# Optimization experiments

Measured on AMD Instinct MI355X. Metric: run time of the kernel, lower is better.

The kernel has to match this reference:

```python
import jax, jax.numpy as jnp
import numpy as np

DT_NS = 8.0
ALPHA, BETA, GAMMA, RISE_W = 0.7, 0.2, 0.1, 0.05
DECAY_TAUS = jnp.array([40.0, 300.0, 230.0, 2.4], dtype=jnp.float32)
RISE_TAUS = jnp.array([5.0, 20.0, 10.0, 2.0], dtype=jnp.float32)
TAIL = 195  # tail window: [peak+5, peak+200)


def setup_inputs() -> dict:
    key = jax.random.key(0)
    k1, k2, k3, k4 = jax.random.split(key, 4)
    B, S, C = 32768, 1024, 4
    return {
        "logits": jax.random.normal(k1, (B, C), dtype=jnp.float32),
        "labels": jax.random.randint(k2, (B,), 0, C, dtype=jnp.int64),
        "waveforms": jax.random.uniform(k3, (B, S), dtype=jnp.float32),
        "amplitudes": jax.random.uniform(k4, (B,), dtype=jnp.float32),
    }


def _masked_mean(vals, valid):
    w = valid.astype(vals.dtype)
    n = jnp.sum(w)
    return jnp.where(n > 0, jnp.sum(vals * w) / jnp.maximum(n, 1.0), 0.0)


def _decay_time_loss(waveforms, pred_cls):
    B, S = waveforms.shape
    peak = jnp.argmax(waveforms, axis=1)                      # (B,)
    valid = peak < S - 20
    # fixed-size tail window starting at peak+5, masked past end of record
    idx = peak[:, None] + 5 + jnp.arange(TAIL)[None, :]       # (B, TAIL)
    in_range = idx < S
    tail = jnp.take_along_axis(waveforms, jnp.minimum(idx, S - 1), axis=1)
    pos = in_range & (tail > 0)                               # positive-sample mask
    w = pos.astype(jnp.float32)
    n_pos = jnp.sum(w, axis=1)
    valid &= n_pos >= 5
    t = (jnp.arange(TAIL, dtype=jnp.float32) * DT_NS)[None, :]
    log_tail = jnp.log(jnp.where(pos, tail, 1.0) + 1e-8)
    n_safe = jnp.maximum(n_pos, 1.0)
    t_mean = jnp.sum(w * t, axis=1) / n_safe
    y_mean = jnp.sum(w * log_tail, axis=1) / n_safe
    dt_c = t - t_mean[:, None]
    num = jnp.sum(w * dt_c * (log_tail - y_mean[:, None]), axis=1)
    den = jnp.sum(w * dt_c * dt_c, axis=1)
    valid &= den > 0
    slope = num / jnp.maximum(den, 1e-30)
    fitted_tau = -1.0 / (slope + 1e-8)
    tau_loss = (fitted_tau - DECAY_TAUS[pred_cls]) ** 2
    return _masked_mean(tau_loss, valid)


def _energy_conservation_loss(waveforms, amplitudes):
    charge = jnp.sum(jnp.maximum(waveforms, 0.0), axis=1)
    ratio = charge / (amplitudes + 1e-8)
    return jnp.var(ratio, ddof=1)  # torch.var default is unbiased


def _rise_time_loss(waveforms, pred_cls):
    B, S = waveforms.shape
    peak = jnp.argmax(waveforms, axis=1)
    amp = jnp.take_along_axis(waveforms, peak[:, None], axis=1)[:, 0]
    valid = peak >= 10
    edge = jnp.arange(S)[None, :] < peak[:, None]             # rising edge mask
    ab10 = edge & (waveforms >= 0.1 * amp[:, None])
    ab90 = edge & (waveforms >= 0.9 * amp[:, None])
    valid &= jnp.any(ab10, axis=1) & jnp.any(ab90, axis=1)
    idx10 = jnp.argmax(ab10, axis=1).astype(jnp.float32)      # first crossing
    idx90 = jnp.argmax(ab90, axis=1).astype(jnp.float32)
    rise = (idx90 - idx10) * DT_NS
    exp_rise = RISE_TAUS[pred_cls]
    rt_loss = jnp.abs(rise - exp_rise) / exp_rise
    return _masked_mean(rt_loss, valid)


def reference(logits, labels, waveforms, amplitudes):
    logp = jax.nn.log_softmax(logits, axis=-1)
    ce = -jnp.mean(jnp.take_along_axis(logp, labels[:, None], axis=1)[:, 0])
    pred_cls = jnp.argmax(logits, axis=1)
    decay = _decay_time_loss(waveforms, pred_cls)
    energy = _energy_conservation_loss(waveforms, amplitudes)
    rise = _rise_time_loss(waveforms, pred_cls)
    total = ALPHA * ce + BETA * decay + GAMMA * energy + RISE_W * rise
    return total, ce, decay, energy, rise
```

## Files before the change

kernel.cpp:

```cpp
#include <hip/hip_runtime.h>
#include <cmath>

#define BROWS 32768
#define SLEN  1024
#define TAILW 195
#define NB1   8192
#define NB2   128
#define PSTRIDE 128

__device__ __constant__ float c_decay_taus[4] = {40.0f, 300.0f, 230.0f, 2.4f};
__device__ __constant__ float c_rise_taus[4]  = {5.0f, 20.0f, 10.0f, 2.0f};

typedef float v2f __attribute__((ext_vector_type(2)));

struct alignas(16) RowStat {
    unsigned nSk;
    unsigned Skk;
    float    csum;
    unsigned pki;
    double   Sy;
    double   Sky;
};

template<int CTRL>
__device__ __forceinline__ unsigned dpp0_u32(unsigned x) {
    return (unsigned)__builtin_amdgcn_update_dpp(0, (int)x, CTRL, 0xf, 0xf, true);
}
template<int CTRL>
__device__ __forceinline__ float dpp0_f32(float x) {
    return __int_as_float(
        __builtin_amdgcn_update_dpp(0, __float_as_int(x), CTRL, 0xf, 0xf, true));
}
template<int CTRL>
__device__ __forceinline__ float dppid_f32(float x) {
    return __int_as_float(__builtin_amdgcn_update_dpp(
        __float_as_int(x), __float_as_int(x), CTRL, 0xf, 0xf, false));
}
template<int CTRL>
__device__ __forceinline__ double dpp0_f64(double x) {
    const int lo = __builtin_amdgcn_update_dpp(0, __double2loint(x), CTRL, 0xf, 0xf, true);
    const int hi = __builtin_amdgcn_update_dpp(0, __double2hiint(x), CTRL, 0xf, 0xf, true);
    return __hiloint2double(hi, lo);
}
#define ROW_SHR1  0x111
#define ROW_SHR2  0x112
#define ROW_SHR4  0x114
#define ROW_SHR8  0x118
#define BCAST15   0x142
#define BCAST31   0x143
#define WSUM_F32(x) { x += dpp0_f32<ROW_SHR1>(x); x += dpp0_f32<ROW_SHR2>(x); \
                      x += dpp0_f32<ROW_SHR4>(x); x += dpp0_f32<ROW_SHR8>(x); \
                      x += dpp0_f32<BCAST15>(x);  x += dpp0_f32<BCAST31>(x); }
#define WSUM_U32(x) { x += dpp0_u32<ROW_SHR1>(x); x += dpp0_u32<ROW_SHR2>(x); \
                      x += dpp0_u32<ROW_SHR4>(x); x += dpp0_u32<ROW_SHR8>(x); \
                      x += dpp0_u32<BCAST15>(x);  x += dpp0_u32<BCAST31>(x); }
#define WSUM_F64(x) { x += dpp0_f64<ROW_SHR1>(x); x += dpp0_f64<ROW_SHR2>(x); \
                      x += dpp0_f64<ROW_SHR4>(x); x += dpp0_f64<ROW_SHR8>(x); \
                      x += dpp0_f64<BCAST15>(x);  x += dpp0_f64<BCAST31>(x); }
#define WMAX_F32(x) { x = fmaxf(x, dppid_f32<ROW_SHR1>(x)); x = fmaxf(x, dppid_f32<ROW_SHR2>(x)); \
                      x = fmaxf(x, dppid_f32<ROW_SHR4>(x)); x = fmaxf(x, dppid_f32<ROW_SHR8>(x)); \
                      x = fmaxf(x, dppid_f32<BCAST15>(x));  x = fmaxf(x, dppid_f32<BCAST31>(x)); }

extern "C" __global__ __launch_bounds__(256, 8)
void physics_rows(const float* __restrict__ wave, RowStat* __restrict__ stats)
{
    const int lane = threadIdx.x & 63;
    const int row  = (blockIdx.x * 256 + (int)threadIdx.x) >> 6;
    const int lane4 = lane * 4;
    const float4* p = reinterpret_cast<const float4*>(wave) + (size_t)row * (SLEN / 4) + lane;

    const float4 c0 = p[0], c1 = p[64], c2 = p[128], c3 = p[192];
    float vals[16] = {c0.x,c0.y,c0.z,c0.w, c1.x,c1.y,c1.z,c1.w,
                      c2.x,c2.y,c2.z,c2.w, c3.x,c3.y,c3.z,c3.w};

    float m0 = fmaxf(fmaxf(vals[0],  vals[1]),  vals[2]);
    float m1 = fmaxf(fmaxf(vals[3],  vals[4]),  vals[5]);
    float m2 = fmaxf(fmaxf(vals[6],  vals[7]),  vals[8]);
    float m3 = fmaxf(fmaxf(vals[9],  vals[10]), vals[11]);
    float m4 = fmaxf(fmaxf(vals[12], vals[13]), fmaxf(vals[14], vals[15]));
    float bm = fmaxf(fmaxf(fmaxf(m0, m1), m2), fmaxf(m3, m4));

    v2f sa = {0.f, 0.f}, sb = {0.f, 0.f};
    #pragma unroll
    for (int k = 0; k < 16; k += 4) {
        v2f p0 = {vals[k],     vals[k + 1]};
        v2f p1 = {vals[k + 2], vals[k + 3]};
        sa += __builtin_elementwise_max(p0, (v2f){0.f, 0.f});
        sb += __builtin_elementwise_max(p1, (v2f){0.f, 0.f});
    }
    const v2f sab = sa + sb;
    float csum = sab.x + sab.y;

    WMAX_F32(bm);
    WSUM_F32(csum);
    const float amp = __int_as_float(
        __builtin_amdgcn_readlane(__float_as_int(bm), 63));

    int peak = SLEN;
    #pragma unroll
    for (int q = 0; q < 4; ++q) {
        bool found = false;
        #pragma unroll
        for (int r = 0; r < 4; ++r) {
            const unsigned long long b = __ballot(vals[q * 4 + r] == amp);
            if (b) {
                peak = min(peak, q * 256 + 4 * (__ffsll(b) - 1) + r);
                found = true;
            }
        }
        if (found) break;
    }
    peak = __builtin_amdgcn_readfirstlane(peak);
    const bool do_decay = (peak < SLEN - 20);
    const int  pm5 = peak + 5;

    const float t10v = 0.1f * amp, t90v = 0.9f * amp;
    int i10 = SLEN, i90 = SLEN;
    const int q_peak = peak >> 8;
    #pragma unroll
    for (int q = 0; q < 4; ++q) {
        if (q > q_peak || (i10 < SLEN && i90 < SLEN)) break;
        const int qb = q * 256;
        unsigned long long m10[4], m90[4];
        #pragma unroll
        for (int r = 0; r < 4; ++r) {
            m10[r] = __ballot(vals[q * 4 + r] >= t10v);
            m90[r] = __ballot(vals[q * 4 + r] >= t90v);
        }
        if (q == q_peak) {
            #pragma unroll
            for (int r = 0; r < 4; ++r) {
                const int cnt = (peak - qb - r + 3) >> 2;
                const unsigned long long lm =
                    (cnt >= 64) ? ~0ull : ((cnt <= 0) ? 0ull : ((1ull << cnt) - 1ull));
                m10[r] &= lm; m90[r] &= lm;
            }
        }
        if (i10 == SLEN) {
            int best = SLEN;
            #pragma unroll
            for (int r = 0; r < 4; ++r)
                if (m10[r]) best = min(best, qb + 4 * (__ffsll(m10[r]) - 1) + r);
            i10 = best;
        }
        if (i90 == SLEN) {
            int best = SLEN;
            #pragma unroll
            for (int r = 0; r < 4; ++r)
                if (m90[r]) best = min(best, qb + 4 * (__ffsll(m90[r]) - 1) + r);
            i90 = best;
        }
    }

    double Sy = 0.0, Sky = 0.0;
    int cnt = 0;
    if (do_decay) {
        #pragma unroll
        for (int q = 0; q < 4; ++q) {
            if (q * 256 + 255 >= pm5 && q * 256 <= pm5 + (TAILW - 1)) {
                #pragma unroll
                for (int r = 0; r < 4; ++r) {
                    const int kk = q * 256 + lane4 + r - pm5;
                    const float w = vals[q * 4 + r];
                    const bool cond = ((unsigned)kk < (unsigned)TAILW) && (w > 0.0f);
                    const float ym = cond ? __logf(w + 1e-8f) : 0.0f;
                    cnt += (int)__popcll(__ballot(cond));
                    const double y64 = (double)ym;
                    Sy += y64;
                    Sky = fma((double)kk, y64, Sky);
                }
            }
        }
    }
    WSUM_F64(Sy);
    WSUM_F64(Sky);

    unsigned out_nSk = 0, out_Skk = 0;
    if (do_decay) {
        const int L = min(TAILW, SLEN - pm5);
        if (cnt == (int)L) {
            const unsigned uL = (unsigned)L;
            const unsigned Sk = uL * (uL - 1u) / 2u;
            out_nSk = uL | (Sk << 16);
            out_Skk = (uL - 1u) * uL * (2u * uL - 1u) / 6u;
        } else {
            unsigned nSk_p = 0, Skk = 0;
            #pragma unroll
            for (int q = 0; q < 4; ++q) {
                if (q * 256 + 255 >= pm5 && q * 256 <= pm5 + (TAILW - 1)) {
                    #pragma unroll
                    for (int r = 0; r < 4; ++r) {
                        const int kk = q * 256 + lane4 + r - pm5;
                        const float w = vals[q * 4 + r];
                        if (((unsigned)kk < (unsigned)TAILW) && (w > 0.0f)) {
                            nSk_p += 1u + ((unsigned)kk << 8);
                            Skk   += (unsigned)(kk * kk);
                        }
                    }
                }
            }
            WSUM_U32(nSk_p);
            WSUM_U32(Skk);
            out_nSk = (nSk_p & 0xFFu) | ((nSk_p >> 8) << 16);
            out_Skk = Skk;
        }
    }

    if (lane == 63) {
        RowStat st;
        st.nSk  = out_nSk;
        st.Skk  = out_Skk;
        st.csum = csum;
        st.pki  = ((unsigned)peak << 22) | ((unsigned)i10 << 11) | (unsigned)i90;
        st.Sy   = Sy;
        st.Sky  = Sky;
        stats[row] = st;
    }
}

extern "C" __global__ __launch_bounds__(256)
void physics_rowfin(const RowStat* __restrict__ stats,
                    const float* __restrict__ logits,
                    const int* __restrict__ labels,
                    const float* __restrict__ amps,
                    double* __restrict__ partials,
                    unsigned* __restrict__ counter,
                    float* __restrict__ out)
{
    const int r    = blockIdx.x * 256 + threadIdx.x;
    const int lane = threadIdx.x & 63;
    const int wid  = threadIdx.x >> 6;

    __shared__ double sm[4][7];
    __shared__ int s_last;

    const RowStat st = stats[r];
    const unsigned n_u  = st.nSk & 0xFFFFu;
    const unsigned Sk_u = st.nSk >> 16;
    const int peak = (int)(st.pki >> 22);
    const int i10  = (int)((st.pki >> 11) & 0x7FFu);
    const int i90  = (int)(st.pki & 0x7FFu);

    const float4 l4 = reinterpret_cast<const float4*>(logits)[r];
    float lg[4] = {l4.x, l4.y, l4.z, l4.w};
    int pred = 0; float pbest = lg[0];
    #pragma unroll
    for (int c = 1; c < 4; ++c) if (lg[c] > pbest) { pbest = lg[c]; pred = c; }
    const float m = fmaxf(fmaxf(lg[0], lg[1]), fmaxf(lg[2], lg[3]));
    const float sexp = expf(lg[0] - m) + expf(lg[1] - m)
                     + expf(lg[2] - m) + expf(lg[3] - m);
    const float lse = m + logf(sexp);
    const double v0 = (double)(lse - lg[labels[r]]);

    double v1 = 0.0, v2 = 0.0;
    if (peak < SLEN - 20 && n_u >= 5u) {
        const double dn  = (double)n_u;
        const double dSk = (double)Sk_u;
        const double num = st.Sky - dSk * st.Sy / dn;
        const double den = 8.0 * ((double)st.Skk - dSk * dSk / dn);
        if (den > 0.0) {
            const double slope = num / fmax(den, 1e-30);
            const double tau   = -1.0 / (slope + 1e-8);
            const double d     = tau - (double)c_decay_taus[pred];
            v1 = d * d; v2 = 1.0;
        }
    }
    double v3 = 0.0, v4 = 0.0;
    if (peak >= 10 && i10 < SLEN && i90 < SLEN) {
        const float rise = (float)(i90 - i10) * 8.0f;
        const float er   = c_rise_taus[pred];
        v3 = (double)(fabsf(rise - er) / er); v4 = 1.0;
    }
    const double ratio = (double)st.csum / ((double)amps[r] + 1e-8);

    double v[7] = {v0, v1, v2, v3, v4, ratio, ratio * ratio};
    #pragma unroll
    for (int i = 0; i < 7; ++i) {
        #pragma unroll
        for (int off = 1; off < 64; off <<= 1)
            v[i] += __shfl_xor(v[i], off, 64);
    }
    if (lane == 0) {
        #pragma unroll
        for (int i = 0; i < 7; ++i) sm[wid][i] = v[i];
    }
    __syncthreads();
    if (threadIdx.x < 7) {
        const int i = threadIdx.x;
        const double t = sm[0][i] + sm[1][i] + sm[2][i] + sm[3][i];
        __hip_atomic_store(&partials[(size_t)i * PSTRIDE + blockIdx.x], t,
                           __ATOMIC_RELAXED, __HIP_MEMORY_SCOPE_AGENT);
    }
    __syncthreads();
    if (threadIdx.x == 0) {
        const unsigned prev = __hip_atomic_fetch_add(counter, 1u,
                                  __ATOMIC_ACQ_REL, __HIP_MEMORY_SCOPE_AGENT);
        s_last = (prev == NB2 - 1) ? 1 : 0;
    }
    __syncthreads();
    if (!s_last) return;

    double loc[7] = {0, 0, 0, 0, 0, 0, 0};
    if (threadIdx.x < PSTRIDE) {
        #pragma unroll
        for (int i = 0; i < 7; ++i)
            loc[i] = __hip_atomic_load(&partials[(size_t)i * PSTRIDE + threadIdx.x],
                                       __ATOMIC_RELAXED, __HIP_MEMORY_SCOPE_AGENT);
    }
    #pragma unroll
    for (int i = 0; i < 7; ++i) {
        #pragma unroll
        for (int off = 1; off < 64; off <<= 1)
            loc[i] += __shfl_xor(loc[i], off, 64);
    }
    __syncthreads();
    if (lane == 0 && wid < 2) {
        #pragma unroll
        for (int i = 0; i < 7; ++i) sm[wid][i] = loc[i];
    }
    __syncthreads();
    if (threadIdx.x == 0) {
        double t[7];
        #pragma unroll
        for (int i = 0; i < 7; ++i) t[i] = sm[0][i] + sm[1][i];
        const double Bn = (double)BROWS;
        const double ce    = t[0] / Bn;
        const double decay = (t[2] > 0.0) ? t[1] / fmax(t[2], 1.0) : 0.0;
        const double rise  = (t[4] > 0.0) ? t[3] / fmax(t[4], 1.0) : 0.0;
        const double var   = (t[6] - t[5] * t[5] / Bn) / (Bn - 1.0);
        const double total = 0.7 * ce + 0.2 * decay + 0.1 * var + 0.05 * rise;
        out[0] = (float)total; out[1] = (float)ce; out[2] = (float)decay;
        out[3] = (float)var;   out[4] = (float)rise;
    }
}

extern "C" void kernel_launch(void* const* d_in, const int* in_sizes, int n_in,
                              void* d_out, int out_size, void* d_ws, size_t ws_size,
                              hipStream_t stream) {
    const float* logits = (const float*)d_in[0];
    const int*   labels = (const int*)d_in[1];
    const float* wave   = (const float*)d_in[2];
    const float* amps   = (const float*)d_in[3];

    RowStat*  stats    = (RowStat*)d_ws;
    double*   partials = (double*)((char*)d_ws + (size_t)BROWS * sizeof(RowStat));
    unsigned* counter  = (unsigned*)((char*)partials + 7 * PSTRIDE * sizeof(double));

    hipMemsetAsync(counter, 0, sizeof(unsigned), stream);
    physics_rows<<<NB1, 256, 0, stream>>>(wave, stats);
    physics_rowfin<<<NB2, 256, 0, stream>>>(stats, logits, labels, amps,
                                            partials, counter, (float*)d_out);
}
```

Before: 39.74 us.

## Process two waveform rows per wavefront to interleave reductions and loads

Each wavefront now handles two rows instead of one. It issues all eight float4 loads up front and interleaves the cross-lane DPP max/sum reductions and the per-row phases of both rows, which halves the number of launched blocks. The aim is more memory-level parallelism and instruction-level overlap of the latency-bound DPP reduction chains. In exchange, register use per thread roughly doubles, and the launch bound drops from 8 to 4 waves per EU, which lowers occupancy.

```diff
diff --git a/kernel.cpp b/kernel.cpp
--- a/kernel.cpp
+++ b/kernel.cpp
@@ -4,7 +4,7 @@
 #define BROWS 32768
 #define SLEN  1024
 #define TAILW 195
-#define NB1   8192
+#define NB1   4096
 #define NB2   128
 #define PSTRIDE 128
 
@@ -61,41 +61,16 @@
                       x = fmaxf(x, dppid_f32<ROW_SHR4>(x)); x = fmaxf(x, dppid_f32<ROW_SHR8>(x)); \
                       x = fmaxf(x, dppid_f32<BCAST15>(x));  x = fmaxf(x, dppid_f32<BCAST31>(x)); }
 
-extern "C" __global__ __launch_bounds__(256, 8)
-void physics_rows(const float* __restrict__ wave, RowStat* __restrict__ stats)
+struct RowRed {
+    int peak, i10, i90, cnt;
+    double Sy, Sky;
+    unsigned nSk_p, Skk;
+    bool slow;
+};
+
+__device__ __forceinline__ void row_phase(const float (&vals)[16], float amp,
+                                          int lane4, RowRed& R)
 {
-    const int lane = threadIdx.x & 63;
-    const int row  = (blockIdx.x * 256 + (int)threadIdx.x) >> 6;
-    const int lane4 = lane * 4;
-    const float4* p = reinterpret_cast<const float4*>(wave) + (size_t)row * (SLEN / 4) + lane;
-
-    const float4 c0 = p[0], c1 = p[64], c2 = p[128], c3 = p[192];
-    float vals[16] = {c0.x,c0.y,c0.z,c0.w, c1.x,c1.y,c1.z,c1.w,
-                      c2.x,c2.y,c2.z,c2.w, c3.x,c3.y,c3.z,c3.w};
-
-    float m0 = fmaxf(fmaxf(vals[0],  vals[1]),  vals[2]);
-    float m1 = fmaxf(fmaxf(vals[3],  vals[4]),  vals[5]);
-    float m2 = fmaxf(fmaxf(vals[6],  vals[7]),  vals[8]);
-    float m3 = fmaxf(fmaxf(vals[9],  vals[10]), vals[11]);
-    float m4 = fmaxf(fmaxf(vals[12], vals[13]), fmaxf(vals[14], vals[15]));
-    float bm = fmaxf(fmaxf(fmaxf(m0, m1), m2), fmaxf(m3, m4));
-
-    v2f sa = {0.f, 0.f}, sb = {0.f, 0.f};
-    #pragma unroll
-    for (int k = 0; k < 16; k += 4) {
-        v2f p0 = {vals[k],     vals[k + 1]};
-        v2f p1 = {vals[k + 2], vals[k + 3]};
-        sa += __builtin_elementwise_max(p0, (v2f){0.f, 0.f});
-        sb += __builtin_elementwise_max(p1, (v2f){0.f, 0.f});
-    }
-    const v2f sab = sa + sb;
-    float csum = sab.x + sab.y;
-
-    WMAX_F32(bm);
-    WSUM_F32(csum);
-    const float amp = __int_as_float(
-        __builtin_amdgcn_readlane(__float_as_int(bm), 63));
-
     int peak = SLEN;
     #pragma unroll
     for (int q = 0; q < 4; ++q) {
@@ -172,19 +147,13 @@
             }
         }
     }
-    WSUM_F64(Sy);
-    WSUM_F64(Sky);
-
-    unsigned out_nSk = 0, out_Skk = 0;
+
+    unsigned nSk_p = 0, Skk = 0;
+    bool slow = false;
     if (do_decay) {
         const int L = min(TAILW, SLEN - pm5);
-        if (cnt == (int)L) {
-            const unsigned uL = (unsigned)L;
-            const unsigned Sk = uL * (uL - 1u) / 2u;
-            out_nSk = uL | (Sk << 16);
-            out_Skk = (uL - 1u) * uL * (2u * uL - 1u) / 6u;
-        } else {
-            unsigned nSk_p = 0, Skk = 0;
+        if (cnt != L) {
+            slow = true;
             #pragma unroll
             for (int q = 0; q < 4; ++q) {
                 if (q * 256 + 255 >= pm5 && q * 256 <= pm5 + (TAILW - 1)) {
@@ -199,22 +168,113 @@
                     }
                 }
             }
+        }
+    }
+    R.peak = peak; R.i10 = i10; R.i90 = i90; R.cnt = cnt;
+    R.Sy = Sy; R.Sky = Sky; R.nSk_p = nSk_p; R.Skk = Skk; R.slow = slow;
+}
+
+__device__ __forceinline__ void row_stat(const RowRed& R, float csum,
+                                         RowStat& st)
+{
+    unsigned out_nSk = 0, out_Skk = 0;
+    if (R.peak < SLEN - 20) {
+        const int L = min(TAILW, SLEN - (R.peak + 5));
+        if (!R.slow) {
+            const unsigned uL = (unsigned)L;
+            const unsigned Sk = uL * (uL - 1u) / 2u;
+            out_nSk = uL | (Sk << 16);
+            out_Skk = (uL - 1u) * uL * (2u * uL - 1u) / 6u;
+        } else {
+            unsigned nSk_p = R.nSk_p, Skk = R.Skk;
             WSUM_U32(nSk_p);
             WSUM_U32(Skk);
             out_nSk = (nSk_p & 0xFFu) | ((nSk_p >> 8) << 16);
             out_Skk = Skk;
         }
     }
+    st.nSk  = out_nSk;
+    st.Skk  = out_Skk;
+    st.csum = csum;
+    st.pki  = ((unsigned)R.peak << 22) | ((unsigned)R.i10 << 11) | (unsigned)R.i90;
+}
+
+extern "C" __global__ __launch_bounds__(256, 4)
+void physics_rows(const float* __restrict__ wave, RowStat* __restrict__ stats)
+{
+    const int lane  = threadIdx.x & 63;
+    const int gwave = (blockIdx.x * 256 + (int)threadIdx.x) >> 6;
+    const int rowA  = gwave * 2;
+    const int rowB  = rowA + 1;
+    const int lane4 = lane * 4;
+    const float4* pA = reinterpret_cast<const float4*>(wave) + (size_t)rowA * (SLEN / 4) + lane;
+    const float4* pB = pA + (SLEN / 4);
+
+    const float4 a0 = pA[0], a1 = pA[64], a2 = pA[128], a3 = pA[192];
+    const float4 b0 = pB[0], b1 = pB[64], b2 = pB[128], b3 = pB[192];
+    float vA[16] = {a0.x,a0.y,a0.z,a0.w, a1.x,a1.y,a1.z,a1.w,
+                    a2.x,a2.y,a2.z,a2.w, a3.x,a3.y,a3.z,a3.w};
+    float vB[16] = {b0.x,b0.y,b0.z,b0.w, b1.x,b1.y,b1.z,b1.w,
+                    b2.x,b2.y,b2.z,b2.w, b3.x,b3.y,b3.z,b3.w};
+
+    float amA0 = fmaxf(fmaxf(vA[0],  vA[1]),  vA[2]);
+    float bmA1 = fmaxf(fmaxf(vA[3],  vA[4]),  vA[5]);
+    float amA2 = fmaxf(fmaxf(vA[6],  vA[7]),  vA[8]);
+    float bmA3 = fmaxf(fmaxf(vA[9],  vA[10]), vA[11]);
+    float amA4 = fmaxf(fmaxf(vA[12], vA[13]), fmaxf(vA[14], vA[15]));
+    float bmA  = fmaxf(fmaxf(fmaxf(amA0, bmA1), amA2), fmaxf(bmA3, amA4));
+
+    float amB0 = fmaxf(fmaxf(vB[0],  vB[1]),  vB[2]);
+    float bmB1 = fmaxf(fmaxf(vB[3],  vB[4]),  vB[5]);
+    float amB2 = fmaxf(fmaxf(vB[6],  vB[7]),  vB[8]);
+    float bmB3 = fmaxf(fmaxf(vB[9],  vB[10]), vB[11]);
+    float amB4 = fmaxf(fmaxf(vB[12], vB[13]), fmaxf(vB[14], vB[15]));
+    float bmB  = fmaxf(fmaxf(fmaxf(amB0, bmB1), amB2), fmaxf(bmB3, amB4));
+
+    v2f saA = {0.f, 0.f}, sbA = {0.f, 0.f}, saB = {0.f, 0.f}, sbB = {0.f, 0.f};
+    #pragma unroll
+    for (int k = 0; k < 16; k += 4) {
+        v2f pa0 = {vA[k],     vA[k + 1]};
+        v2f pa1 = {vA[k + 2], vA[k + 3]};
+        v2f pb0 = {vB[k],     vB[k + 1]};
+        v2f pb1 = {vB[k + 2], vB[k + 3]};
+        saA += __builtin_elementwise_max(pa0, (v2f){0.f, 0.f});
+        sbA += __builtin_elementwise_max(pa1, (v2f){0.f, 0.f});
+        saB += __builtin_elementwise_max(pb0, (v2f){0.f, 0.f});
+        sbB += __builtin_elementwise_max(pb1, (v2f){0.f, 0.f});
+    }
+    const v2f sabA = saA + sbA;
+    const v2f sabB = saB + sbB;
+    float csumA = sabA.x + sabA.y;
+    float csumB = sabB.x + sabB.y;
+
+    WMAX_F32(bmA);
+    WMAX_F32(bmB);
+    WSUM_F32(csumA);
+    WSUM_F32(csumB);
+    const float ampA = __int_as_float(
+        __builtin_amdgcn_readlane(__float_as_int(bmA), 63));
+    const float ampB = __int_as_float(
+        __builtin_amdgcn_readlane(__float_as_int(bmB), 63));
+
+    RowRed RA, RB;
+    row_phase(vA, ampA, lane4, RA);
+    row_phase(vB, ampB, lane4, RB);
+
+    WSUM_F64(RA.Sy);
+    WSUM_F64(RA.Sky);
+    WSUM_F64(RB.Sy);
+    WSUM_F64(RB.Sky);
+
+    RowStat stA, stB;
+    row_stat(RA, csumA, stA);
+    row_stat(RB, csumB, stB);
+    stA.Sy = RA.Sy;  stA.Sky = RA.Sky;
+    stB.Sy = RB.Sy;  stB.Sky = RB.Sky;
 
     if (lane == 63) {
-        RowStat st;
-        st.nSk  = out_nSk;
-        st.Skk  = out_Skk;
-        st.csum = csum;
-        st.pki  = ((unsigned)peak << 22) | ((unsigned)i10 << 11) | (unsigned)i90;
-        st.Sy   = Sy;
-        st.Sky  = Sky;
-        stats[row] = st;
+        stats[rowA] = stA;
+        stats[rowB] = stB;
     }
 }
 
```

Result: slower. 42.38 us (+6.6%).
